# Optimization experiments

Measured on AMD Instinct MI355X. Metric: run time of the kernel, lower is better.

## Reference

```python
import jax, jax.numpy as jnp
import numpy as np

N_FP, EMB, L_CONV, C, L_LIN = 10000, 64, 5, 256, 2
N_NODES, N_EDGES, N_GRAPHS = 40000, 640000, 128


def setup_inputs() -> dict:
    key = jax.random.key(0)
    ks = jax.random.split(key, 16)
    s = 0.05
    inp = {
        "x_idx": jax.random.randint(ks[0], (N_NODES,), 0, N_FP),
        "edge_index": jax.random.randint(ks[1], (2, N_EDGES), 0, N_NODES),
        "batch": jnp.sort(jax.random.randint(ks[2], (N_NODES,), 0, N_GRAPHS)),
        # embedding table
        "embed": jax.random.normal(ks[3], (N_FP, EMB), jnp.float32) * s,
        # in_conv: GraphConv(EMB -> C)
        "w_rel0": jax.random.normal(ks[4], (EMB, C), jnp.float32) * s,
        "b_rel0": jnp.zeros((C,), jnp.float32),
        "w_root0": jax.random.normal(ks[5], (EMB, C), jnp.float32) * s,
        # stacked GraphConv(C -> C) x L_CONV
        "w_rel": jax.random.normal(ks[6], (L_CONV, C, C), jnp.float32) * s,
        "b_rel": jnp.zeros((L_CONV, C), jnp.float32),
        "w_root": jax.random.normal(ks[7], (L_CONV, C, C), jnp.float32) * s,
        # lin0: C -> 2C
        "w_lin0": jax.random.normal(ks[8], (C, 2 * C), jnp.float32) * s,
        "b_lin0": jnp.zeros((2 * C,), jnp.float32),
        # lin layers: 2C -> 2C x L_LIN
        "w_lin": jax.random.normal(ks[9], (L_LIN, 2 * C, 2 * C), jnp.float32) * s,
        "b_lin": jnp.zeros((L_LIN, 2 * C), jnp.float32),
        # out: 2C -> 1
        "w_out": jax.random.normal(ks[10], (2 * C, 1), jnp.float32) * s,
        "b_out": jnp.zeros((1,), jnp.float32),
    }
    return inp


def _graph_conv(x, src, dst, w_rel, b_rel, w_root):
    # PyG GraphConv (aggr='add'): lin_rel(sum_{j in N(i)} x_j) + lin_root(x_i)
    agg = jax.ops.segment_sum(x[src], dst, num_segments=N_NODES)  # [N, in]
    return agg @ w_rel + b_rel + x @ w_root


def reference(x_idx, edge_index, batch, embed, w_rel0, b_rel0, w_root0,
              w_rel, b_rel, w_root, w_lin0, b_lin0, w_lin, b_lin, w_out, b_out):
    src, dst = edge_index[0], edge_index[1]
    x = embed[x_idx]                                            # [N, EMB]
    x = jax.nn.relu(_graph_conv(x, src, dst, w_rel0, b_rel0, w_root0))
    for i in range(L_CONV):
        x = jax.nn.relu(_graph_conv(x, src, dst, w_rel[i], b_rel[i], w_root[i]))
    g = jax.ops.segment_sum(x, batch, num_segments=N_GRAPHS)    # global_add_pool [G, C]
    h = jax.nn.relu(g @ w_lin0 + b_lin0)                        # [G, 2C]
    for i in range(L_LIN):
        h = jax.nn.relu(h @ w_lin[i] + b_lin[i])
    return h @ w_out + b_out                                    # [G, 1]
```

## Files before the change

### kernel.cpp

```cpp
#include <hip/hip_runtime.h>
#include <hip/hip_bf16.h>

#define N_FP 10000
#define EMB 64
#define L_CONV 5
#define CC 256
#define HID 512
#define N_NODES 40000
#define N_EDGES 640000
#define N_GRAPHS 128
#define MP 40064
#define SCAN_BLOCKS 157
#define POOL_CHUNK 128
#define POOL_BLOCKS 313
#define WSCALE 0.25f
#define UNSCALE 4096.0f

typedef __attribute__((ext_vector_type(8))) _Float16 half8;
typedef __attribute__((ext_vector_type(4))) float f32x4;

__device__ inline float h2f(unsigned int bits16) {
  return (float)__builtin_bit_cast(_Float16, (unsigned short)bits16);
}
__device__ inline unsigned short f2h(float x) {
  return __builtin_bit_cast(unsigned short, (_Float16)x);
}

__global__ void zero_ints(int* __restrict__ p, int n) {
  int i = blockIdx.x * blockDim.x + threadIdx.x;
  if (i < n) p[i] = 0;
}

__global__ void count_deg(const int* __restrict__ dst, int* __restrict__ deg) {
  int e = blockIdx.x * blockDim.x + threadIdx.x;
  if (e < N_EDGES) atomicAdd(&deg[dst[e]], 1);
}

__global__ void scan_partial(const int* __restrict__ deg, int* __restrict__ partial) {
  __shared__ int sm[256];
  int t = threadIdx.x;
  int idx = blockIdx.x * 256 + t;
  sm[t] = (idx < N_NODES) ? deg[idx] : 0;
  __syncthreads();
  for (int off = 128; off > 0; off >>= 1) {
    if (t < off) sm[t] += sm[t + off];
    __syncthreads();
  }
  if (t == 0) partial[blockIdx.x] = sm[0];
}

__global__ void scan_top(int* __restrict__ partial) {
  __shared__ int sm[256];
  int t = threadIdx.x;
  int own = (t < SCAN_BLOCKS) ? partial[t] : 0;
  sm[t] = own;
  __syncthreads();
  for (int off = 1; off < 256; off <<= 1) {
    int v = (t >= off) ? sm[t - off] : 0;
    __syncthreads();
    sm[t] += v;
    __syncthreads();
  }
  if (t < SCAN_BLOCKS) partial[t] = sm[t] - own;
}

__global__ void scan_final(const int* __restrict__ deg, const int* __restrict__ partial,
                           int* __restrict__ offs, int* __restrict__ cursor) {
  __shared__ int sm[256];
  int t = threadIdx.x;
  int idx = blockIdx.x * 256 + t;
  int own = (idx < N_NODES) ? deg[idx] : 0;
  sm[t] = own;
  __syncthreads();
  for (int off = 1; off < 256; off <<= 1) {
    int v = (t >= off) ? sm[t - off] : 0;
    __syncthreads();
    sm[t] += v;
    __syncthreads();
  }
  int excl = sm[t] - own + partial[blockIdx.x];
  if (idx < N_NODES) { offs[idx] = excl; cursor[idx] = excl; }
  if (idx == N_NODES - 1) offs[N_NODES] = excl + own;
}

__global__ void scatter_edges(const int* __restrict__ src, const int* __restrict__ dst,
                              int* __restrict__ cursor, int* __restrict__ csr) {
  int e = blockIdx.x * blockDim.x + threadIdx.x;
  if (e < N_EDGES) {
    int d = dst[e];
    int slot = atomicAdd(&cursor[d], 1);
    csr[slot] = src[e];
  }
}

__global__ void transpose_scale_f16(const float* __restrict__ W, unsigned short* __restrict__ out,
                                    int K, int N, float scale) {
  int i = blockIdx.x * 256 + threadIdx.x;
  if (i >= K * N) return;
  int k = i / N, n = i % N;
  out[(size_t)n * K + k] = f2h(W[i] * scale);
}

__global__ void transpose_scale_all_f16(const float* __restrict__ W, unsigned short* __restrict__ out,
                                        float scale) {
  int i = blockIdx.x * 256 + threadIdx.x;
  if (i >= L_CONV * CC * CC) return;
  int l = i >> 16;
  int rem = i & 65535;
  int k = rem >> 8, n = rem & 255;
  out[((size_t)l << 16) + n * CC + k] = f2h(W[i] * scale);
}

__global__ void embed_gather_f16(const int* __restrict__ x_idx, const float* __restrict__ emb,
                                 unsigned short* __restrict__ x0) {
  int i = blockIdx.x * 256 + threadIdx.x;
  int n = i >> 6;
  int c = i & 63;
  x0[i] = f2h(emb[(size_t)x_idx[n] * EMB + c]);
}

__global__ void aggregate64_f16(const unsigned short* __restrict__ xp, const int* __restrict__ offs,
                                const int* __restrict__ csr, unsigned short* __restrict__ aggp) {
  int wid = (blockIdx.x * blockDim.x + threadIdx.x) >> 6;
  int lane = threadIdx.x & 63;
  if (wid >= N_NODES) return;
  int gr = lane >> 3;
  int sl = lane & 7;
  int s = offs[wid], e = offs[wid + 1];
  float a0 = 0.f, a1 = 0.f, a2 = 0.f, a3 = 0.f, a4 = 0.f, a5 = 0.f, a6 = 0.f, a7 = 0.f;
  for (int j = s + gr; j < e; j += 8) {
    int sv = csr[j];
    uint4 v = *(const uint4*)(xp + (size_t)sv * 64 + sl * 8);
    a0 += h2f(v.x & 0xffff); a1 += h2f(v.x >> 16);
    a2 += h2f(v.y & 0xffff); a3 += h2f(v.y >> 16);
    a4 += h2f(v.z & 0xffff); a5 += h2f(v.z >> 16);
    a6 += h2f(v.w & 0xffff); a7 += h2f(v.w >> 16);
  }
#pragma unroll
  for (int off = 32; off >= 8; off >>= 1) {
    a0 += __shfl_down(a0, off); a1 += __shfl_down(a1, off);
    a2 += __shfl_down(a2, off); a3 += __shfl_down(a3, off);
    a4 += __shfl_down(a4, off); a5 += __shfl_down(a5, off);
    a6 += __shfl_down(a6, off); a7 += __shfl_down(a7, off);
  }
  if (lane < 8) {
    uint4 o;
    o.x = (unsigned int)f2h(a0) | ((unsigned int)f2h(a1) << 16);
    o.y = (unsigned int)f2h(a2) | ((unsigned int)f2h(a3) << 16);
    o.z = (unsigned int)f2h(a4) | ((unsigned int)f2h(a5) << 16);
    o.w = (unsigned int)f2h(a6) | ((unsigned int)f2h(a7) << 16);
    *(uint4*)(aggp + (size_t)wid * 64 + lane * 8) = o;
  }
}

__global__ void aggregate256_f16(const unsigned short* __restrict__ xp, const int* __restrict__ offs,
                                 const int* __restrict__ csr, unsigned short* __restrict__ aggp) {
  int wid = (blockIdx.x * blockDim.x + threadIdx.x) >> 6;
  int lane = threadIdx.x & 63;
  if (wid >= N_NODES) return;
  int es = lane >> 4;
  int sl = lane & 15;
  int s = offs[wid], e = offs[wid + 1];
  float a[16];
#pragma unroll
  for (int i = 0; i < 16; ++i) a[i] = 0.f;
  for (int j = s + es; j < e; j += 4) {
    int sv = csr[j];
    uint4 v0 = *(const uint4*)(xp + (size_t)sv * 256 + sl * 8);
    uint4 v1 = *(const uint4*)(xp + (size_t)sv * 256 + 128 + sl * 8);
    a[0] += h2f(v0.x & 0xffff); a[1] += h2f(v0.x >> 16);
    a[2] += h2f(v0.y & 0xffff); a[3] += h2f(v0.y >> 16);
    a[4] += h2f(v0.z & 0xffff); a[5] += h2f(v0.z >> 16);
    a[6] += h2f(v0.w & 0xffff); a[7] += h2f(v0.w >> 16);
    a[8]  += h2f(v1.x & 0xffff); a[9]  += h2f(v1.x >> 16);
    a[10] += h2f(v1.y & 0xffff); a[11] += h2f(v1.y >> 16);
    a[12] += h2f(v1.z & 0xffff); a[13] += h2f(v1.z >> 16);
    a[14] += h2f(v1.w & 0xffff); a[15] += h2f(v1.w >> 16);
  }
#pragma unroll
  for (int off = 32; off >= 16; off >>= 1) {
#pragma unroll
    for (int i = 0; i < 16; ++i) a[i] += __shfl_down(a[i], off);
  }
  if (lane < 16) {
    uint4 o0, o1;
    o0.x = (unsigned int)f2h(a[0]) | ((unsigned int)f2h(a[1]) << 16);
    o0.y = (unsigned int)f2h(a[2]) | ((unsigned int)f2h(a[3]) << 16);
    o0.z = (unsigned int)f2h(a[4]) | ((unsigned int)f2h(a[5]) << 16);
    o0.w = (unsigned int)f2h(a[6]) | ((unsigned int)f2h(a[7]) << 16);
    o1.x = (unsigned int)f2h(a[8])  | ((unsigned int)f2h(a[9])  << 16);
    o1.y = (unsigned int)f2h(a[10]) | ((unsigned int)f2h(a[11]) << 16);
    o1.z = (unsigned int)f2h(a[12]) | ((unsigned int)f2h(a[13]) << 16);
    o1.w = (unsigned int)f2h(a[14]) | ((unsigned int)f2h(a[15]) << 16);
    *(uint4*)(aggp + (size_t)wid * 256 + sl * 8) = o0;
    *(uint4*)(aggp + (size_t)wid * 256 + 128 + sl * 8) = o1;
  }
}

template<int K1>
__global__ __launch_bounds__(256)
void gemm_conv_f16(const unsigned short* __restrict__ A1, const unsigned short* __restrict__ A2,
                   const unsigned short* __restrict__ W1, const unsigned short* __restrict__ W2,
                   const float* __restrict__ bias, float bscale,
                   unsigned short* __restrict__ outp) {
  __shared__ __align__(16) unsigned short As[128 * 72];
  __shared__ __align__(16) unsigned short Bs[128 * 72];

  const int t = threadIdx.x;
  const int row0 = blockIdx.x * 128;
  const int col0 = blockIdx.y * 128;
  const int lane = t & 63;
  const int wave = t >> 6;
  const int wm = wave >> 1;
  const int wn = wave & 1;
  const int fr = lane & 15;
  const int fg = lane >> 4;

  f32x4 acc[4][4];
#pragma unroll
  for (int i = 0; i < 4; ++i)
#pragma unroll
    for (int j = 0; j < 4; ++j) acc[i][j] = (f32x4)(0.f);

  for (int srcp = 0; srcp < 2; ++srcp) {
    const unsigned short* __restrict__ A = srcp ? A2 : A1;
    const unsigned short* __restrict__ W = srcp ? W2 : W1;
    for (int ks = 0; ks < K1 / 64; ++ks) {
      const int kb = ks * 64;
#pragma unroll
      for (int i = 0; i < 4; ++i) {
        int idx = t + i * 256;
        int r = idx >> 3;
        int q = idx & 7;
        *(uint4*)(As + r * 72 + q * 8) =
            *(const uint4*)(A + (size_t)(row0 + r) * K1 + kb + q * 8);
        *(uint4*)(Bs + r * 72 + q * 8) =
            *(const uint4*)(W + (size_t)(col0 + r) * K1 + kb + q * 8);
      }
      __syncthreads();

#pragma unroll
      for (int sub = 0; sub < 2; ++sub) {
        half8 ah[4];
#pragma unroll
        for (int mi = 0; mi < 4; ++mi) {
          int r = wm * 64 + mi * 16 + fr;
          ah[mi] = *(const half8*)(As + r * 72 + sub * 32 + fg * 8);
        }
#pragma unroll
        for (int ni = 0; ni < 4; ++ni) {
          int rn = wn * 64 + ni * 16 + fr;
          half8 bh = *(const half8*)(Bs + rn * 72 + sub * 32 + fg * 8);
#pragma unroll
          for (int mi = 0; mi < 4; ++mi) {
            acc[mi][ni] = __builtin_amdgcn_mfma_f32_16x16x32_f16(ah[mi], bh, acc[mi][ni], 0, 0, 0);
          }
        }
      }
      __syncthreads();
    }
  }

#pragma unroll
  for (int ni = 0; ni < 4; ++ni) {
    int col = col0 + wn * 64 + ni * 16 + fr;
    float b = bias[col] * bscale;
#pragma unroll
    for (int mi = 0; mi < 4; ++mi) {
#pragma unroll
      for (int r = 0; r < 4; ++r) {
        int row = row0 + wm * 64 + mi * 16 + fg * 4 + r;
        float v = fmaxf(acc[mi][ni][r] + b, 0.f);
        outp[(size_t)row * 256 + col] = f2h(v);
      }
    }
  }
}

__global__ void pool_chunk_f16(const unsigned short* __restrict__ xp, const int* __restrict__ batch,
                               float* __restrict__ gb) {
  int wave = threadIdx.x >> 6;
  int lane = threadIdx.x & 63;
  int c0 = blockIdx.x * POOL_CHUNK;
  int c1 = min(c0 + POOL_CHUNK, N_NODES);
  float a0 = 0.f, a1 = 0.f, a2 = 0.f, a3 = 0.f;
  int curb = -1;
  for (int i = c0 + wave; i < c1; i += 4) {
    int b = batch[i];
    if (b != curb) {
      if (curb >= 0) {
        float* g = gb + (size_t)curb * 256 + lane * 4;
        atomicAdd(g + 0, a0 * UNSCALE); atomicAdd(g + 1, a1 * UNSCALE);
        atomicAdd(g + 2, a2 * UNSCALE); atomicAdd(g + 3, a3 * UNSCALE);
      }
      curb = b;
      a0 = a1 = a2 = a3 = 0.f;
    }
    uint2 v = *(const uint2*)(xp + (size_t)i * 256 + lane * 4);
    a0 += h2f(v.x & 0xffff); a1 += h2f(v.x >> 16);
    a2 += h2f(v.y & 0xffff); a3 += h2f(v.y >> 16);
  }
  if (curb >= 0) {
    float* g = gb + (size_t)curb * 256 + lane * 4;
    atomicAdd(g + 0, a0 * UNSCALE); atomicAdd(g + 1, a1 * UNSCALE);
    atomicAdd(g + 2, a2 * UNSCALE); atomicAdd(g + 3, a3 * UNSCALE);
  }
}

template<int K, int N, bool RELU>
__global__ __launch_bounds__(512)
void mlp_linear(const float* __restrict__ A, const float* __restrict__ W,
                const float* __restrict__ bias, float* __restrict__ out) {
  __shared__ float a[4][K];
  const int t = threadIdx.x;
  const int g0 = blockIdx.x * 4;
  const int n0 = blockIdx.y * 128;
#pragma unroll
  for (int i = 0; i < (4 * K) / 512; ++i) {
    int idx = t + i * 512;
    a[idx / K][idx % K] = A[(size_t)g0 * K + idx];
  }
  __syncthreads();
  const int gl = t >> 7;
  const int n = n0 + (t & 127);
  const float* __restrict__ ar = a[gl];
  const float* __restrict__ w = W + n;
  float acc = bias[n];
#pragma unroll 8
  for (int k = 0; k < K; ++k) acc = fmaf(ar[k], w[(size_t)k * N], acc);
  if (RELU) acc = fmaxf(acc, 0.f);
  out[(size_t)(g0 + gl) * N + n] = acc;
}

__global__ void out_layer(const float* __restrict__ h, const float* __restrict__ w,
                          const float* __restrict__ b, float* __restrict__ out) {
  int g = blockIdx.x;
  int t = threadIdx.x;
  float acc = 0.f;
#pragma unroll 4
  for (int k = t; k < HID; k += 64) acc = fmaf(h[(size_t)g * HID + k], w[k], acc);
  for (int off = 32; off > 0; off >>= 1) acc += __shfl_down(acc, off);
  if (t == 0) out[g] = acc + b[0];
}

extern "C" void kernel_launch(void* const* d_in, const int* in_sizes, int n_in,
                              void* d_out, int out_size, void* d_ws, size_t ws_size,
                              hipStream_t stream) {
  const int* x_idx = (const int*)d_in[0];
  const int* edge_index = (const int*)d_in[1];
  const int* batch = (const int*)d_in[2];
  const float* embed = (const float*)d_in[3];
  const float* w_rel0 = (const float*)d_in[4];
  const float* b_rel0 = (const float*)d_in[5];
  const float* w_root0 = (const float*)d_in[6];
  const float* w_rel = (const float*)d_in[7];
  const float* b_rel = (const float*)d_in[8];
  const float* w_root = (const float*)d_in[9];
  const float* w_lin0 = (const float*)d_in[10];
  const float* b_lin0 = (const float*)d_in[11];
  const float* w_lin = (const float*)d_in[12];
  const float* b_lin = (const float*)d_in[13];
  const float* w_out = (const float*)d_in[14];
  const float* b_out = (const float*)d_in[15];
  float* out = (float*)d_out;

  const int* src = edge_index;
  const int* dst = edge_index + N_EDGES;

  char* ws = (char*)d_ws;
  size_t off = 0;
  auto alloc = [&](size_t bytes) -> void* {
    void* p = ws + off;
    off = (off + bytes + 255) & ~(size_t)255;
    return p;
  };
  int* deg     = (int*)alloc((size_t)N_NODES * 4);
  int* cursor  = (int*)alloc((size_t)N_NODES * 4);
  int* offs    = (int*)alloc((size_t)(N_NODES + 1) * 4);
  int* partial = (int*)alloc((size_t)SCAN_BLOCKS * 4);
  int* csr     = (int*)alloc((size_t)N_EDGES * 4);
  unsigned short* x0  = (unsigned short*)alloc((size_t)MP * EMB * 2);
  unsigned short* agg = (unsigned short*)alloc((size_t)MP * CC * 2);
  unsigned short* xA  = (unsigned short*)alloc((size_t)MP * CC * 2);
  unsigned short* xB  = (unsigned short*)alloc((size_t)MP * CC * 2);
  unsigned short* w0rel_t  = (unsigned short*)alloc((size_t)CC * EMB * 2);
  unsigned short* w0root_t = (unsigned short*)alloc((size_t)CC * EMB * 2);
  unsigned short* wrel_t  = (unsigned short*)alloc((size_t)L_CONV * CC * CC * 2);
  unsigned short* wroot_t = (unsigned short*)alloc((size_t)L_CONV * CC * CC * 2);
  float* gb = (float*)alloc((size_t)N_GRAPHS * CC * 4);
  float* h1 = (float*)alloc((size_t)N_GRAPHS * HID * 4);
  float* h2 = (float*)alloc((size_t)N_GRAPHS * HID * 4);

  zero_ints<<<(N_NODES + 255) / 256, 256, 0, stream>>>(deg, N_NODES);
  count_deg<<<N_EDGES / 256, 256, 0, stream>>>(dst, deg);
  scan_partial<<<SCAN_BLOCKS, 256, 0, stream>>>(deg, partial);
  scan_top<<<1, 256, 0, stream>>>(partial);
  scan_final<<<SCAN_BLOCKS, 256, 0, stream>>>(deg, partial, offs, cursor);
  scatter_edges<<<N_EDGES / 256, 256, 0, stream>>>(src, dst, cursor, csr);

  transpose_scale_f16<<<(EMB * CC + 255) / 256, 256, 0, stream>>>(w_rel0, w0rel_t, EMB, CC, WSCALE);
  transpose_scale_f16<<<(EMB * CC + 255) / 256, 256, 0, stream>>>(w_root0, w0root_t, EMB, CC, WSCALE);
  transpose_scale_all_f16<<<(L_CONV * CC * CC + 255) / 256, 256, 0, stream>>>(w_rel, wrel_t, WSCALE);
  transpose_scale_all_f16<<<(L_CONV * CC * CC + 255) / 256, 256, 0, stream>>>(w_root, wroot_t, WSCALE);

  embed_gather_f16<<<(N_NODES * EMB) / 256, 256, 0, stream>>>(x_idx, embed, x0);

  dim3 gemm_grid(MP / 128, CC / 128);

  aggregate64_f16<<<(N_NODES + 3) / 4, 256, 0, stream>>>(x0, offs, csr, agg);
  gemm_conv_f16<EMB><<<gemm_grid, 256, 0, stream>>>(agg, x0, w0rel_t, w0root_t,
                                                    b_rel0, 0.25f, xA);

  const float bscales[L_CONV] = {0.0625f, 0.015625f, 3.90625e-3f, 9.765625e-4f, 2.44140625e-4f};
  unsigned short *cur = xA, *nxt = xB;
  for (int l = 0; l < L_CONV; ++l) {
    size_t o = (size_t)l * CC * CC;
    aggregate256_f16<<<(N_NODES + 3) / 4, 256, 0, stream>>>(cur, offs, csr, agg);
    gemm_conv_f16<CC><<<gemm_grid, 256, 0, stream>>>(agg, cur, wrel_t + o, wroot_t + o,
                                                     b_rel + (size_t)l * CC, bscales[l], nxt);
    unsigned short* tmp = cur; cur = nxt; nxt = tmp;
  }

  zero_ints<<<(N_GRAPHS * CC) / 256, 256, 0, stream>>>((int*)gb, N_GRAPHS * CC);
  pool_chunk_f16<<<POOL_BLOCKS, 256, 0, stream>>>(cur, batch, gb);
  mlp_linear<CC, HID, true><<<dim3(N_GRAPHS / 4, HID / 128), 512, 0, stream>>>(gb, w_lin0, b_lin0, h1);
  mlp_linear<HID, HID, true><<<dim3(N_GRAPHS / 4, HID / 128), 512, 0, stream>>>(h1, w_lin, b_lin, h2);
  mlp_linear<HID, HID, true><<<dim3(N_GRAPHS / 4, HID / 128), 512, 0, stream>>>(h2, w_lin + HID * HID, b_lin + HID, h1);
  out_layer<<<N_GRAPHS, 64, 0, stream>>>(h1, w_out, b_out, out);
}
```

Baseline: 545.4 us.

## Register-prefetch next GEMM tile and unroll edge aggregation loops by two

The conv GEMM now loads the next K-tile from global memory into registers while the MFMA loop runs on the current tile in shared memory. This hides global load latency behind compute. The two aggregation kernels are also unrolled to issue two independent neighbor gathers per iteration, which raises memory-level parallelism. The cost is more registers per thread, which may lower occupancy.

```diff
diff --git a/kernel.cpp b/kernel.cpp
--- a/kernel.cpp
+++ b/kernel.cpp
@@ -128,7 +128,22 @@
   int sl = lane & 7;
   int s = offs[wid], e = offs[wid + 1];
   float a0 = 0.f, a1 = 0.f, a2 = 0.f, a3 = 0.f, a4 = 0.f, a5 = 0.f, a6 = 0.f, a7 = 0.f;
-  for (int j = s + gr; j < e; j += 8) {
+  int j = s + gr;
+  for (; j + 8 < e; j += 16) {
+    int sv0 = csr[j];
+    int sv1 = csr[j + 8];
+    uint4 v0 = *(const uint4*)(xp + (size_t)sv0 * 64 + sl * 8);
+    uint4 v1 = *(const uint4*)(xp + (size_t)sv1 * 64 + sl * 8);
+    a0 += h2f(v0.x & 0xffff); a1 += h2f(v0.x >> 16);
+    a2 += h2f(v0.y & 0xffff); a3 += h2f(v0.y >> 16);
+    a4 += h2f(v0.z & 0xffff); a5 += h2f(v0.z >> 16);
+    a6 += h2f(v0.w & 0xffff); a7 += h2f(v0.w >> 16);
+    a0 += h2f(v1.x & 0xffff); a1 += h2f(v1.x >> 16);
+    a2 += h2f(v1.y & 0xffff); a3 += h2f(v1.y >> 16);
+    a4 += h2f(v1.z & 0xffff); a5 += h2f(v1.z >> 16);
+    a6 += h2f(v1.w & 0xffff); a7 += h2f(v1.w >> 16);
+  }
+  if (j < e) {
     int sv = csr[j];
     uint4 v = *(const uint4*)(xp + (size_t)sv * 64 + sl * 8);
     a0 += h2f(v.x & 0xffff); a1 += h2f(v.x >> 16);
@@ -164,18 +179,43 @@
   float a[16];
 #pragma unroll
   for (int i = 0; i < 16; ++i) a[i] = 0.f;
-  for (int j = s + es; j < e; j += 4) {
+  int j = s + es;
+  for (; j + 4 < e; j += 8) {
+    int sv0 = csr[j];
+    int sv1 = csr[j + 4];
+    uint4 v0a = *(const uint4*)(xp + (size_t)sv0 * 256 + sl * 8);
+    uint4 v0b = *(const uint4*)(xp + (size_t)sv0 * 256 + 128 + sl * 8);
+    uint4 v1a = *(const uint4*)(xp + (size_t)sv1 * 256 + sl * 8);
+    uint4 v1b = *(const uint4*)(xp + (size_t)sv1 * 256 + 128 + sl * 8);
+    a[0] += h2f(v0a.x & 0xffff); a[1] += h2f(v0a.x >> 16);
+    a[2] += h2f(v0a.y & 0xffff); a[3] += h2f(v0a.y >> 16);
+    a[4] += h2f(v0a.z & 0xffff); a[5] += h2f(v0a.z >> 16);
+    a[6] += h2f(v0a.w & 0xffff); a[7] += h2f(v0a.w >> 16);
+    a[8]  += h2f(v0b.x & 0xffff); a[9]  += h2f(v0b.x >> 16);
+    a[10] += h2f(v0b.y & 0xffff); a[11] += h2f(v0b.y >> 16);
+    a[12] += h2f(v0b.z & 0xffff); a[13] += h2f(v0b.z >> 16);
+    a[14] += h2f(v0b.w & 0xffff); a[15] += h2f(v0b.w >> 16);
+    a[0] += h2f(v1a.x & 0xffff); a[1] += h2f(v1a.x >> 16);
+    a[2] += h2f(v1a.y & 0xffff); a[3] += h2f(v1a.y >> 16);
+    a[4] += h2f(v1a.z & 0xffff); a[5] += h2f(v1a.z >> 16);
+    a[6] += h2f(v1a.w & 0xffff); a[7] += h2f(v1a.w >> 16);
+    a[8]  += h2f(v1b.x & 0xffff); a[9]  += h2f(v1b.x >> 16);
+    a[10] += h2f(v1b.y & 0xffff); a[11] += h2f(v1b.y >> 16);
+    a[12] += h2f(v1b.z & 0xffff); a[13] += h2f(v1b.z >> 16);
+    a[14] += h2f(v1b.w & 0xffff); a[15] += h2f(v1b.w >> 16);
+  }
+  if (j < e) {
     int sv = csr[j];
-    uint4 v0 = *(const uint4*)(xp + (size_t)sv * 256 + sl * 8);
-    uint4 v1 = *(const uint4*)(xp + (size_t)sv * 256 + 128 + sl * 8);
-    a[0] += h2f(v0.x & 0xffff); a[1] += h2f(v0.x >> 16);
-    a[2] += h2f(v0.y & 0xffff); a[3] += h2f(v0.y >> 16);
-    a[4] += h2f(v0.z & 0xffff); a[5] += h2f(v0.z >> 16);
-    a[6] += h2f(v0.w & 0xffff); a[7] += h2f(v0.w >> 16);
-    a[8]  += h2f(v1.x & 0xffff); a[9]  += h2f(v1.x >> 16);
-    a[10] += h2f(v1.y & 0xffff); a[11] += h2f(v1.y >> 16);
-    a[12] += h2f(v1.z & 0xffff); a[13] += h2f(v1.z >> 16);
-    a[14] += h2f(v1.w & 0xffff); a[15] += h2f(v1.w >> 16);
+    uint4 va = *(const uint4*)(xp + (size_t)sv * 256 + sl * 8);
+    uint4 vb = *(const uint4*)(xp + (size_t)sv * 256 + 128 + sl * 8);
+    a[0] += h2f(va.x & 0xffff); a[1] += h2f(va.x >> 16);
+    a[2] += h2f(va.y & 0xffff); a[3] += h2f(va.y >> 16);
+    a[4] += h2f(va.z & 0xffff); a[5] += h2f(va.z >> 16);
+    a[6] += h2f(va.w & 0xffff); a[7] += h2f(va.w >> 16);
+    a[8]  += h2f(vb.x & 0xffff); a[9]  += h2f(vb.x >> 16);
+    a[10] += h2f(vb.y & 0xffff); a[11] += h2f(vb.y >> 16);
+    a[12] += h2f(vb.z & 0xffff); a[13] += h2f(vb.z >> 16);
+    a[14] += h2f(vb.w & 0xffff); a[15] += h2f(vb.w >> 16);
   }
 #pragma unroll
   for (int off = 32; off >= 16; off >>= 1) {
@@ -205,6 +245,8 @@
                    unsigned short* __restrict__ outp) {
   __shared__ __align__(16) unsigned short As[128 * 72];
   __shared__ __align__(16) unsigned short Bs[128 * 72];
+  constexpr int NK = K1 / 64;
+  constexpr int NT = 2 * NK;
 
   const int t = threadIdx.x;
   const int row0 = blockIdx.x * 128;
@@ -215,6 +257,8 @@
   const int wn = wave & 1;
   const int fr = lane & 15;
   const int fg = lane >> 4;
+  const int sr = t >> 3;
+  const int sq = t & 7;
 
   f32x4 acc[4][4];
 #pragma unroll
@@ -222,43 +266,49 @@
 #pragma unroll
     for (int j = 0; j < 4; ++j) acc[i][j] = (f32x4)(0.f);
 
-  for (int srcp = 0; srcp < 2; ++srcp) {
-    const unsigned short* __restrict__ A = srcp ? A2 : A1;
-    const unsigned short* __restrict__ W = srcp ? W2 : W1;
-    for (int ks = 0; ks < K1 / 64; ++ks) {
-      const int kb = ks * 64;
-#pragma unroll
-      for (int i = 0; i < 4; ++i) {
-        int idx = t + i * 256;
-        int r = idx >> 3;
-        int q = idx & 7;
-        *(uint4*)(As + r * 72 + q * 8) =
-            *(const uint4*)(A + (size_t)(row0 + r) * K1 + kb + q * 8);
-        *(uint4*)(Bs + r * 72 + q * 8) =
-            *(const uint4*)(W + (size_t)(col0 + r) * K1 + kb + q * 8);
+  uint4 ra[4], rb[4];
+  auto gload = [&](int it) {
+    const unsigned short* __restrict__ A = (it < NK) ? A1 : A2;
+    const unsigned short* __restrict__ W = (it < NK) ? W1 : W2;
+    const int kb = ((it < NK) ? it : it - NK) * 64;
+#pragma unroll
+    for (int i = 0; i < 4; ++i) {
+      int r = sr + i * 32;
+      ra[i] = *(const uint4*)(A + (size_t)(row0 + r) * K1 + kb + sq * 8);
+      rb[i] = *(const uint4*)(W + (size_t)(col0 + r) * K1 + kb + sq * 8);
+    }
+  };
+
+  gload(0);
+  for (int it = 0; it < NT; ++it) {
+#pragma unroll
+    for (int i = 0; i < 4; ++i) {
+      int r = sr + i * 32;
+      *(uint4*)(As + r * 72 + sq * 8) = ra[i];
+      *(uint4*)(Bs + r * 72 + sq * 8) = rb[i];
+    }
+    __syncthreads();
+    if (it + 1 < NT) gload(it + 1);
+
+#pragma unroll
+    for (int sub = 0; sub < 2; ++sub) {
+      half8 ah[4];
+#pragma unroll
+      for (int mi = 0; mi < 4; ++mi) {
+        int r = wm * 64 + mi * 16 + fr;
+        ah[mi] = *(const half8*)(As + r * 72 + sub * 32 + fg * 8);
       }
-      __syncthreads();
-
-#pragma unroll
-      for (int sub = 0; sub < 2; ++sub) {
-        half8 ah[4];
+#pragma unroll
+      for (int ni = 0; ni < 4; ++ni) {
+        int rn = wn * 64 + ni * 16 + fr;
+        half8 bh = *(const half8*)(Bs + rn * 72 + sub * 32 + fg * 8);
 #pragma unroll
         for (int mi = 0; mi < 4; ++mi) {
-          int r = wm * 64 + mi * 16 + fr;
-          ah[mi] = *(const half8*)(As + r * 72 + sub * 32 + fg * 8);
-        }
-#pragma unroll
-        for (int ni = 0; ni < 4; ++ni) {
-          int rn = wn * 64 + ni * 16 + fr;
-          half8 bh = *(const half8*)(Bs + rn * 72 + sub * 32 + fg * 8);
-#pragma unroll
-          for (int mi = 0; mi < 4; ++mi) {
-            acc[mi][ni] = __builtin_amdgcn_mfma_f32_16x16x32_f16(ah[mi], bh, acc[mi][ni], 0, 0, 0);
-          }
+          acc[mi][ni] = __builtin_amdgcn_mfma_f32_16x16x32_f16(ah[mi], bh, acc[mi][ni], 0, 0, 0);
         }
       }
-      __syncthreads();
     }
+    __syncthreads();
   }
 
 #pragma unroll
```

New measurement: 732.9 us. +34.4%, slower.

## Slice node features into 32-channel planes for cache-friendly aggregation and GEMM

Applied to the files above, without the earlier changes.

Stores node features as column slices of 32 halves (64 bytes per node per slice), so each aggregation block gathers from a single slice whose working set fits better in cache. The GEMM loads A from the sliced layout directly into LDS using global_load_lds with an XOR swizzle instead of padding, and writes its output through shared memory back into the sliced layout. Pooling is adapted to the new layout. The cost is more aggregation blocks that each re-read the CSR offsets and indices, plus narrower 64-byte row accesses.

```diff
diff --git a/kernel.cpp b/kernel.cpp
--- a/kernel.cpp
+++ b/kernel.cpp
@@ -116,84 +116,49 @@
   int i = blockIdx.x * 256 + threadIdx.x;
   int n = i >> 6;
   int c = i & 63;
-  x0[i] = f2h(emb[(size_t)x_idx[n] * EMB + c]);
-}
-
-__global__ void aggregate64_f16(const unsigned short* __restrict__ xp, const int* __restrict__ offs,
-                                const int* __restrict__ csr, unsigned short* __restrict__ aggp) {
-  int wid = (blockIdx.x * blockDim.x + threadIdx.x) >> 6;
-  int lane = threadIdx.x & 63;
-  if (wid >= N_NODES) return;
-  int gr = lane >> 3;
-  int sl = lane & 7;
-  int s = offs[wid], e = offs[wid + 1];
-  float a0 = 0.f, a1 = 0.f, a2 = 0.f, a3 = 0.f, a4 = 0.f, a5 = 0.f, a6 = 0.f, a7 = 0.f;
-  for (int j = s + gr; j < e; j += 8) {
-    int sv = csr[j];
-    uint4 v = *(const uint4*)(xp + (size_t)sv * 64 + sl * 8);
-    a0 += h2f(v.x & 0xffff); a1 += h2f(v.x >> 16);
-    a2 += h2f(v.y & 0xffff); a3 += h2f(v.y >> 16);
-    a4 += h2f(v.z & 0xffff); a5 += h2f(v.z >> 16);
-    a6 += h2f(v.w & 0xffff); a7 += h2f(v.w >> 16);
-  }
-#pragma unroll
-  for (int off = 32; off >= 8; off >>= 1) {
-    a0 += __shfl_down(a0, off); a1 += __shfl_down(a1, off);
-    a2 += __shfl_down(a2, off); a3 += __shfl_down(a3, off);
-    a4 += __shfl_down(a4, off); a5 += __shfl_down(a5, off);
-    a6 += __shfl_down(a6, off); a7 += __shfl_down(a7, off);
-  }
-  if (lane < 8) {
-    uint4 o;
-    o.x = (unsigned int)f2h(a0) | ((unsigned int)f2h(a1) << 16);
-    o.y = (unsigned int)f2h(a2) | ((unsigned int)f2h(a3) << 16);
-    o.z = (unsigned int)f2h(a4) | ((unsigned int)f2h(a5) << 16);
-    o.w = (unsigned int)f2h(a6) | ((unsigned int)f2h(a7) << 16);
-    *(uint4*)(aggp + (size_t)wid * 64 + lane * 8) = o;
-  }
-}
-
-__global__ void aggregate256_f16(const unsigned short* __restrict__ xp, const int* __restrict__ offs,
-                                 const int* __restrict__ csr, unsigned short* __restrict__ aggp) {
-  int wid = (blockIdx.x * blockDim.x + threadIdx.x) >> 6;
-  int lane = threadIdx.x & 63;
-  if (wid >= N_NODES) return;
-  int es = lane >> 4;
-  int sl = lane & 15;
-  int s = offs[wid], e = offs[wid + 1];
-  float a[16];
-#pragma unroll
-  for (int i = 0; i < 16; ++i) a[i] = 0.f;
-  for (int j = s + es; j < e; j += 4) {
-    int sv = csr[j];
-    uint4 v0 = *(const uint4*)(xp + (size_t)sv * 256 + sl * 8);
-    uint4 v1 = *(const uint4*)(xp + (size_t)sv * 256 + 128 + sl * 8);
-    a[0] += h2f(v0.x & 0xffff); a[1] += h2f(v0.x >> 16);
-    a[2] += h2f(v0.y & 0xffff); a[3] += h2f(v0.y >> 16);
-    a[4] += h2f(v0.z & 0xffff); a[5] += h2f(v0.z >> 16);
-    a[6] += h2f(v0.w & 0xffff); a[7] += h2f(v0.w >> 16);
-    a[8]  += h2f(v1.x & 0xffff); a[9]  += h2f(v1.x >> 16);
-    a[10] += h2f(v1.y & 0xffff); a[11] += h2f(v1.y >> 16);
-    a[12] += h2f(v1.z & 0xffff); a[13] += h2f(v1.z >> 16);
-    a[14] += h2f(v1.w & 0xffff); a[15] += h2f(v1.w >> 16);
-  }
-#pragma unroll
-  for (int off = 32; off >= 16; off >>= 1) {
-#pragma unroll
-    for (int i = 0; i < 16; ++i) a[i] += __shfl_down(a[i], off);
-  }
-  if (lane < 16) {
-    uint4 o0, o1;
-    o0.x = (unsigned int)f2h(a[0]) | ((unsigned int)f2h(a[1]) << 16);
-    o0.y = (unsigned int)f2h(a[2]) | ((unsigned int)f2h(a[3]) << 16);
-    o0.z = (unsigned int)f2h(a[4]) | ((unsigned int)f2h(a[5]) << 16);
-    o0.w = (unsigned int)f2h(a[6]) | ((unsigned int)f2h(a[7]) << 16);
-    o1.x = (unsigned int)f2h(a[8])  | ((unsigned int)f2h(a[9])  << 16);
-    o1.y = (unsigned int)f2h(a[10]) | ((unsigned int)f2h(a[11]) << 16);
-    o1.z = (unsigned int)f2h(a[12]) | ((unsigned int)f2h(a[13]) << 16);
-    o1.w = (unsigned int)f2h(a[14]) | ((unsigned int)f2h(a[15]) << 16);
-    *(uint4*)(aggp + (size_t)wid * 256 + sl * 8) = o0;
-    *(uint4*)(aggp + (size_t)wid * 256 + 128 + sl * 8) = o1;
+  x0[(size_t)(c >> 5) * (MP * 32) + (size_t)n * 32 + (c & 31)] =
+      f2h(emb[(size_t)x_idx[n] * EMB + c]);
+}
+
+template<int NSLICE>
+__global__ __launch_bounds__(256)
+void aggregate_sliced(const unsigned short* __restrict__ xs, const int* __restrict__ offs,
+                      const int* __restrict__ csr, unsigned short* __restrict__ aggs) {
+  const int slice = blockIdx.x % NSLICE;
+  const int chunk = blockIdx.x / NSLICE;
+  const unsigned short* __restrict__ xp = xs + (size_t)slice * (MP * 32);
+  unsigned short* __restrict__ ap = aggs + (size_t)slice * (MP * 32);
+  const int wave = threadIdx.x >> 6;
+  const int lane = threadIdx.x & 63;
+  const int q = lane & 3;
+  const int es = lane >> 2;
+  const int n1 = min(chunk * 128 + 128, N_NODES);
+  for (int n = chunk * 128 + wave; n < n1; n += 4) {
+    int s = offs[n], e = offs[n + 1];
+    float a0 = 0.f, a1 = 0.f, a2 = 0.f, a3 = 0.f, a4 = 0.f, a5 = 0.f, a6 = 0.f, a7 = 0.f;
+    for (int j = s + es; j < e; j += 16) {
+      int sv = __builtin_nontemporal_load(csr + j);
+      uint4 v = *(const uint4*)(xp + (size_t)sv * 32 + q * 8);
+      a0 += h2f(v.x & 0xffff); a1 += h2f(v.x >> 16);
+      a2 += h2f(v.y & 0xffff); a3 += h2f(v.y >> 16);
+      a4 += h2f(v.z & 0xffff); a5 += h2f(v.z >> 16);
+      a6 += h2f(v.w & 0xffff); a7 += h2f(v.w >> 16);
+    }
+#pragma unroll
+    for (int off = 4; off <= 32; off <<= 1) {
+      a0 += __shfl_down(a0, off); a1 += __shfl_down(a1, off);
+      a2 += __shfl_down(a2, off); a3 += __shfl_down(a3, off);
+      a4 += __shfl_down(a4, off); a5 += __shfl_down(a5, off);
+      a6 += __shfl_down(a6, off); a7 += __shfl_down(a7, off);
+    }
+    if (lane < 4) {
+      uint4 o;
+      o.x = (unsigned int)f2h(a0) | ((unsigned int)f2h(a1) << 16);
+      o.y = (unsigned int)f2h(a2) | ((unsigned int)f2h(a3) << 16);
+      o.z = (unsigned int)f2h(a4) | ((unsigned int)f2h(a5) << 16);
+      o.w = (unsigned int)f2h(a6) | ((unsigned int)f2h(a7) << 16);
+      *(uint4*)(ap + (size_t)n * 32 + lane * 8) = o;
+    }
   }
 }
 
@@ -203,8 +168,9 @@
                    const unsigned short* __restrict__ W1, const unsigned short* __restrict__ W2,
                    const float* __restrict__ bias, float bscale,
                    unsigned short* __restrict__ outp) {
-  __shared__ __align__(16) unsigned short As[128 * 72];
-  __shared__ __align__(16) unsigned short Bs[128 * 72];
+  __shared__ __align__(16) unsigned short smem[2 * 128 * 64];
+  unsigned short* As = smem;
+  unsigned short* Bs = smem + 128 * 64;
 
   const int t = threadIdx.x;
   const int row0 = blockIdx.x * 128;
@@ -229,28 +195,35 @@
       const int kb = ks * 64;
 #pragma unroll
       for (int i = 0; i < 4; ++i) {
-        int idx = t + i * 256;
-        int r = idx >> 3;
-        int q = idx & 7;
-        *(uint4*)(As + r * 72 + q * 8) =
-            *(const uint4*)(A + (size_t)(row0 + r) * K1 + kb + q * 8);
-        *(uint4*)(Bs + r * 72 + q * 8) =
-            *(const uint4*)(W + (size_t)(col0 + r) * K1 + kb + q * 8);
+        int P = i * 256 + t;
+        int r = P >> 3;
+        int q = (P & 7) ^ (r & 7);
+        int ch = kb + q * 8;
+        const unsigned short* ga =
+            A + (size_t)(ch >> 5) * (MP * 32) + (size_t)(row0 + r) * 32 + (ch & 31);
+        const unsigned short* gw = W + (size_t)(col0 + r) * K1 + kb + q * 8;
+        __builtin_amdgcn_global_load_lds(
+            (const __attribute__((address_space(1))) unsigned int*)ga,
+            (__attribute__((address_space(3))) unsigned int*)(As + P * 8), 16, 0, 0);
+        __builtin_amdgcn_global_load_lds(
+            (const __attribute__((address_space(1))) unsigned int*)gw,
+            (__attribute__((address_space(3))) unsigned int*)(Bs + P * 8), 16, 0, 0);
       }
       __syncthreads();
 
 #pragma unroll
       for (int sub = 0; sub < 2; ++sub) {
+        const int q = sub * 4 + fg;
         half8 ah[4];
 #pragma unroll
         for (int mi = 0; mi < 4; ++mi) {
-          int r = wm * 64 + mi * 16 + fr;
-          ah[mi] = *(const half8*)(As + r * 72 + sub * 32 + fg * 8);
+          int ar = wm * 64 + mi * 16 + fr;
+          ah[mi] = *(const half8*)(As + (ar * 8 + (q ^ (ar & 7))) * 8);
         }
 #pragma unroll
         for (int ni = 0; ni < 4; ++ni) {
           int rn = wn * 64 + ni * 16 + fr;
-          half8 bh = *(const half8*)(Bs + rn * 72 + sub * 32 + fg * 8);
+          half8 bh = *(const half8*)(Bs + (rn * 8 + (q ^ (rn & 7))) * 8);
 #pragma unroll
           for (int mi = 0; mi < 4; ++mi) {
             acc[mi][ni] = __builtin_amdgcn_mfma_f32_16x16x32_f16(ah[mi], bh, acc[mi][ni], 0, 0, 0);
@@ -263,17 +236,26 @@
 
 #pragma unroll
   for (int ni = 0; ni < 4; ++ni) {
-    int col = col0 + wn * 64 + ni * 16 + fr;
-    float b = bias[col] * bscale;
+    int col = wn * 64 + ni * 16 + fr;
+    float b = bias[col0 + col] * bscale;
 #pragma unroll
     for (int mi = 0; mi < 4; ++mi) {
 #pragma unroll
       for (int r = 0; r < 4; ++r) {
-        int row = row0 + wm * 64 + mi * 16 + fg * 4 + r;
+        int row = wm * 64 + mi * 16 + fg * 4 + r;
         float v = fmaxf(acc[mi][ni][r] + b, 0.f);
-        outp[(size_t)row * 256 + col] = f2h(v);
+        smem[row * 128 + col] = f2h(v);
       }
     }
+  }
+  __syncthreads();
+#pragma unroll
+  for (int p = 0; p < 8; ++p) {
+    int idx = p * 2048 + t * 8;
+    int row = idx >> 7;
+    int c = col0 + (idx & 127);
+    *(uint4*)(outp + (size_t)(c >> 5) * (MP * 32) + (size_t)(row0 + row) * 32 + (c & 31)) =
+        *(const uint4*)(smem + idx);
   }
 }
 
@@ -281,6 +263,7 @@
                                float* __restrict__ gb) {
   int wave = threadIdx.x >> 6;
   int lane = threadIdx.x & 63;
+  const unsigned short* base = xp + (size_t)(lane >> 3) * (MP * 32) + (lane & 7) * 4;
   int c0 = blockIdx.x * POOL_CHUNK;
   int c1 = min(c0 + POOL_CHUNK, N_NODES);
   float a0 = 0.f, a1 = 0.f, a2 = 0.f, a3 = 0.f;
@@ -296,7 +279,7 @@
       curb = b;
       a0 = a1 = a2 = a3 = 0.f;
     }
-    uint2 v = *(const uint2*)(xp + (size_t)i * 256 + lane * 4);
+    uint2 v = *(const uint2*)(base + (size_t)i * 32);
     a0 += h2f(v.x & 0xffff); a1 += h2f(v.x >> 16);
     a2 += h2f(v.y & 0xffff); a3 += h2f(v.y >> 16);
   }
@@ -407,7 +390,7 @@
 
   dim3 gemm_grid(MP / 128, CC / 128);
 
-  aggregate64_f16<<<(N_NODES + 3) / 4, 256, 0, stream>>>(x0, offs, csr, agg);
+  aggregate_sliced<2><<<POOL_BLOCKS * 2, 256, 0, stream>>>(x0, offs, csr, agg);
   gemm_conv_f16<EMB><<<gemm_grid, 256, 0, stream>>>(agg, x0, w0rel_t, w0root_t,
                                                     b_rel0, 0.25f, xA);
 
@@ -415,7 +398,7 @@
   unsigned short *cur = xA, *nxt = xB;
   for (int l = 0; l < L_CONV; ++l) {
     size_t o = (size_t)l * CC * CC;
-    aggregate256_f16<<<(N_NODES + 3) / 4, 256, 0, stream>>>(cur, offs, csr, agg);
+    aggregate_sliced<8><<<POOL_BLOCKS * 8, 256, 0, stream>>>(cur, offs, csr, agg);
     gemm_conv_f16<CC><<<gemm_grid, 256, 0, stream>>>(agg, cur, wrel_t + o, wroot_t + o,
                                                      b_rel + (size_t)l * CC, bscales[l], nxt);
     unsigned short* tmp = cur; cur = nxt; nxt = tmp;
```

Measured after the change: 1.039 ms. 1.91x slower.
